# Performance work log

Hardware: AMD Instinct MI355X
Metric: run time of the kernel (lower is better)

The kernel has to match this reference:

```python
import jax, jax.numpy as jnp
import numpy as np

B, C, H, W = 16, 2048, 64, 64
PROJ_DIM, ATTN_DIM = 128, 64
MAX_SAMPLES = 64
TEMPERATURE = 0.1
BASE_TEMPERATURE = 0.07
SIM_THRESHOLD = 0.7
LOSS_WEIGHT = 0.1
BN_EPS = 1e-5


def setup_inputs() -> dict:
    key = jax.random.key(0)
    ks = jax.random.split(key, 12)
    inp = {
        "feats": jax.random.normal(ks[0], (B, C, H, W), dtype=jnp.float32),
        "labels": jax.random.randint(ks[1], (B, H, W), 0, 2, dtype=jnp.int64),
        # projection: Conv1x1(C->128) -> BN -> ReLU -> Conv1x1(128->128)
        "W1": jax.random.normal(ks[2], (PROJ_DIM, C), dtype=jnp.float32) * (1.0 / np.sqrt(C)),
        "b1": jnp.zeros((PROJ_DIM,), jnp.float32),
        "gamma": jnp.ones((PROJ_DIM,), jnp.float32),
        "beta": jnp.zeros((PROJ_DIM,), jnp.float32),
        "W2": jax.random.normal(ks[3], (PROJ_DIM, PROJ_DIM), dtype=jnp.float32) * (1.0 / np.sqrt(PROJ_DIM)),
        "b2": jnp.zeros((PROJ_DIM,), jnp.float32),
        # pixel attention: Conv1x1(C->64) -> ReLU -> Conv1x1(64->1) -> Sigmoid
        "Wa1": jax.random.normal(ks[4], (ATTN_DIM, C), dtype=jnp.float32) * (1.0 / np.sqrt(C)),
        "ba1": jnp.zeros((ATTN_DIM,), jnp.float32),
        "Wa2": jax.random.normal(ks[5], (1, ATTN_DIM), dtype=jnp.float32) * (1.0 / np.sqrt(ATTN_DIM)),
        "ba2": jnp.zeros((1,), jnp.float32),
    }
    return inp


def _conv1x1(x, Wt, b):  # x: [B,Cin,H,W], Wt: [Cout,Cin]
    return jnp.einsum("bchw,oc->bohw", x, Wt) + b[None, :, None, None]


def _batchnorm_train(x, gamma, beta):  # per-channel stats over (B,H,W)
    mean = x.mean(axis=(0, 2, 3), keepdims=True)
    var = x.var(axis=(0, 2, 3), keepdims=True)
    xn = (x - mean) * jax.lax.rsqrt(var + BN_EPS)
    return xn * gamma[None, :, None, None] + beta[None, :, None, None]


def _single_image_loss(f, lab, w):
    # f: [HW,128] L2-normalized, lab: [HW] int, w: [HW]
    valid = lab == 1
    # deterministic stand-in for randperm sampling: first MAX_SAMPLES valid pixels
    idx = jnp.nonzero(valid, size=MAX_SAMPLES, fill_value=0)[0]
    tf = f[idx]                       # [S,128]
    tw = w[idx]                       # [S]
    sim = (tf @ tf.T) / TEMPERATURE   # [S,S]
    pos = (sim > SIM_THRESHOLD) & ~jnp.eye(MAX_SAMPLES, dtype=bool)
    exp_sim = jnp.exp(sim)
    denom = exp_sim.sum(axis=1)       # [S]
    log_prob = jnp.log(exp_sim / denom[:, None] + 1e-10)
    pair_w = tw[:, None] * tw[None, :]
    loss = -(TEMPERATURE / BASE_TEMPERATURE) * jnp.sum(
        jnp.where(pos, pair_w * log_prob, 0.0)
    )
    return loss / tw.sum()


def reference(feats, labels, W1, b1, gamma, beta, W2, b2, Wa1, ba1, Wa2, ba2):
    # projection head
    h = _conv1x1(feats, W1, b1)
    h = jax.nn.relu(_batchnorm_train(h, gamma, beta))
    proj = _conv1x1(h, W2, b2)                      # [B,128,H,W]
    # pixel attention
    a = jax.nn.relu(_conv1x1(feats, Wa1, ba1))
    attn = jax.nn.sigmoid(_conv1x1(a, Wa2, ba2))    # [B,1,H,W]

    f = proj.transpose(0, 2, 3, 1).reshape(B, H * W, PROJ_DIM)
    f = f / jnp.clip(jnp.linalg.norm(f, axis=-1, keepdims=True), 1e-12)
    wts = attn.transpose(0, 2, 3, 1).reshape(B, H * W)
    labs = labels.reshape(B, H * W)

    losses = jax.vmap(_single_image_loss)(f, labs, wts)  # [B]
    return jnp.mean(losses) * LOSS_WEIGHT
```

## Files before the change

kernel.cpp:

```cpp
#include <hip/hip_runtime.h>
#include <hip/hip_bf16.h>
#include <math.h>

#define B_ 16
#define C_ 2048
#define HW_ 4096
#define NPIX_ 65536
#define PD_ 128
#define AD_ 64
#define S_ 64
#define BN_EPS_ 1e-5f
#define TEMP_ 0.1f
#define BTEMP_ 0.07f
#define THR_ 0.7f
#define LW_ 0.1f

typedef __attribute__((ext_vector_type(8))) short short8;
typedef __attribute__((ext_vector_type(4))) float floatx4;

__device__ __forceinline__ unsigned short f2bf(float x) {
    unsigned int u = __float_as_uint(x);
    u += 0x7fffu + ((u >> 16) & 1u);
    return (unsigned short)(u >> 16);
}

__global__ void zero_kernel(float* xsum, float* ssq, float* out) {
    int t = threadIdx.x;
    for (int i = t; i < C_; i += 256) xsum[i] = 0.0f;
    if (t < PD_) ssq[t] = 0.0f;
    if (t == 0) out[0] = 0.0f;
}

__global__ void prep_kernel(const float* __restrict__ W1, const float* __restrict__ Wa1,
                            const float* __restrict__ W2, float* __restrict__ W1t,
                            float* __restrict__ Wa1t, float* __restrict__ W2t,
                            uint4* __restrict__ Bpk) {
    int g = blockIdx.x * blockDim.x + threadIdx.x;
    if (g < C_ * PD_) { int k = g >> 7, c = g & 127; W1t[g] = W1[c * C_ + k]; }
    if (g < C_ * AD_) { int k = g >> 6, j = g & 63;  Wa1t[g] = Wa1[j * C_ + k]; }
    if (g < PD_ * PD_){ int k = g >> 7, c = g & 127; W2t[g] = W2[c * PD_ + k]; }
    if (g < 64 * 4 * PD_) {
        int kc = g >> 9, q = (g >> 7) & 3, c = g & 127;
        const float* src = W1 + (size_t)c * C_ + kc * 32 + q * 8;
        unsigned int w[4];
#pragma unroll
        for (int h = 0; h < 4; h++) {
            unsigned int lo = f2bf(src[2 * h]);
            unsigned int hi = f2bf(src[2 * h + 1]);
            w[h] = lo | (hi << 16);
        }
        Bpk[g] = make_uint4(w[0], w[1], w[2], w[3]);
    }
}

#define NKC_ 64
__global__ __launch_bounds__(256) void fused_stats_kernel(const float* __restrict__ feats,
                                                          const uint4* __restrict__ Bpk,
                                                          float* __restrict__ xsum,
                                                          float* __restrict__ ssq) {
    __shared__ uint4 bw[2][512];
    __shared__ float lxsum[C_];
    __shared__ float red[4][PD_];

    int t = threadIdx.x;
    for (int i = t; i < C_; i += 256) lxsum[i] = 0.0f;

    int tile = blockIdx.x;
    int b = tile >> 6;
    int hw0 = (tile & 63) << 6;
    int wave = t >> 6, lane = t & 63;
    int qd = lane >> 4, ln16 = lane & 15;
    const float* fb = feats + (size_t)b * C_ * HW_ + (hw0 + wave * 16 + ln16);

    floatx4 acc[8];
#pragma unroll
    for (int nt = 0; nt < 8; nt++) acc[nt] = (floatx4)0.0f;

    bw[0][t] = Bpk[t];
    bw[0][t + 256] = Bpk[t + 256];
    __syncthreads();

    for (int kc = 0; kc < NKC_; kc++) {
        int cur = kc & 1;
        uint4 u0, u1;
        if (kc + 1 < NKC_) {
            u0 = Bpk[(kc + 1) * 512 + t];
            u1 = Bpk[(kc + 1) * 512 + t + 256];
        }
        const float* pk = fb + (size_t)(kc * 32 + qd * 8) * HW_;
        float av[8];
#pragma unroll
        for (int j = 0; j < 8; j++) av[j] = pk[(size_t)j * HW_];

#pragma unroll
        for (int j = 0; j < 8; j++) {
            float v = av[j];
            v += __shfl_xor(v, 1, 64);
            v += __shfl_xor(v, 2, 64);
            v += __shfl_xor(v, 4, 64);
            v += __shfl_xor(v, 8, 64);
            if (ln16 == 0) atomicAdd(&lxsum[kc * 32 + qd * 8 + j], v);
        }

        short8 afrag;
#pragma unroll
        for (int j = 0; j < 8; j++) afrag[j] = (short)f2bf(av[j]);

#pragma unroll
        for (int nt = 0; nt < 8; nt++) {
            short8 bfrag = *reinterpret_cast<const short8*>(&bw[cur][qd * 128 + nt * 16 + ln16]);
            acc[nt] = __builtin_amdgcn_mfma_f32_16x16x32_bf16(afrag, bfrag, acc[nt], 0, 0, 0);
        }

        if (kc + 1 < NKC_) {
            bw[cur ^ 1][t] = u0;
            bw[cur ^ 1][t + 256] = u1;
        }
        __syncthreads();
    }

#pragma unroll
    for (int nt = 0; nt < 8; nt++) {
        float s = 0.0f;
#pragma unroll
        for (int r = 0; r < 4; r++) s = fmaf(acc[nt][r], acc[nt][r], s);
        s += __shfl_xor(s, 16, 64);
        s += __shfl_xor(s, 32, 64);
        if (qd == 0) red[wave][nt * 16 + ln16] = s;
    }
    __syncthreads();
    if (t < PD_) {
        float tot = red[0][t] + red[1][t] + red[2][t] + red[3][t];
        atomicAdd(&ssq[t], tot);
    }
    for (int i = t; i < C_; i += 256) atomicAdd(&xsum[i], lxsum[i]);
}

__global__ __launch_bounds__(256) void stats_kernel(const float* __restrict__ W1,
                                                    const float* __restrict__ xsum,
                                                    const float* __restrict__ ssq,
                                                    const float* __restrict__ b1,
                                                    float* __restrict__ mean,
                                                    float* __restrict__ invstd) {
    int c = blockIdx.x, t = threadIdx.x;
    const float* row = W1 + (size_t)c * C_;
    float acc = 0.0f;
    for (int k = t; k < C_; k += 256) acc = fmaf(row[k], xsum[k], acc);
    for (int o = 32; o > 0; o >>= 1) acc += __shfl_down(acc, o, 64);
    __shared__ float red[4];
    if ((t & 63) == 0) red[t >> 6] = acc;
    __syncthreads();
    if (t == 0) {
        float m0 = (red[0] + red[1] + red[2] + red[3]) * (1.0f / NPIX_);
        float var = ssq[c] * (1.0f / NPIX_) - m0 * m0;
        mean[c] = m0 + b1[c];
        invstd[c] = rsqrtf(var + BN_EPS_);
    }
}

__global__ __launch_bounds__(256) void find_kernel(const int* __restrict__ labels,
                                                   int* __restrict__ idx) {
    __shared__ int cnt[256];
    __shared__ int pref[257];
    int b = blockIdx.x, t = threadIdx.x;
    const int* lb = labels + b * HW_;
    int base = t * 16, c0 = 0;
    for (int i = 0; i < 16; i++) c0 += (lb[base + i] == 1);
    cnt[t] = c0;
    __syncthreads();
    if (t == 0) {
        int s = 0;
        for (int i = 0; i < 256; i++) { pref[i] = s; s += cnt[i]; }
        pref[256] = s;
    }
    __syncthreads();
    int r = pref[t];
    for (int i = 0; i < 16; i++) {
        if (lb[base + i] == 1) {
            if (r < S_) idx[b * S_ + r] = base + i;
            r++;
        }
    }
    if (t == 0) {
        for (int k = pref[256]; k < S_; k++) idx[b * S_ + k] = 0;
    }
}

__global__ __launch_bounds__(256) void sample_kernel(
        const float* __restrict__ feats, const float* __restrict__ W1t,
        const float* __restrict__ b1, const float* __restrict__ mean,
        const float* __restrict__ invstd, const float* __restrict__ gamma,
        const float* __restrict__ beta, const float* __restrict__ W2t,
        const float* __restrict__ b2, const float* __restrict__ Wa1t,
        const float* __restrict__ ba1, const float* __restrict__ Wa2,
        const float* __restrict__ ba2, const int* __restrict__ idx,
        float* __restrict__ projs, float* __restrict__ tw) {
    __shared__ float x[C_];
    __shared__ float rh[PD_];
    __shared__ float av[AD_];
    int s = blockIdx.x;
    int b = s >> 6;
    int pix = idx[s];
    int t = threadIdx.x;
    const float* fb = feats + (size_t)b * C_ * HW_ + pix;
    for (int c = t; c < C_; c += 256) x[c] = fb[(size_t)c * HW_];
    __syncthreads();
    if (t < PD_) {
        float h = b1[t];
        for (int k = 0; k < C_; k++) h = fmaf(W1t[k * PD_ + t], x[k], h);
        float r = (h - mean[t]) * invstd[t] * gamma[t] + beta[t];
        rh[t] = r > 0.0f ? r : 0.0f;
    } else if (t < PD_ + AD_) {
        int j = t - PD_;
        float a = ba1[j];
        for (int k = 0; k < C_; k++) a = fmaf(Wa1t[k * AD_ + j], x[k], a);
        av[j] = a > 0.0f ? a : 0.0f;
    }
    __syncthreads();
    if (t < PD_) {
        float p = b2[t];
        for (int j = 0; j < PD_; j++) p = fmaf(W2t[j * PD_ + t], rh[j], p);
        projs[s * PD_ + t] = p;
    } else if (t == PD_) {
        float a2 = ba2[0];
        for (int j = 0; j < AD_; j++) a2 = fmaf(Wa2[j], av[j], a2);
        tw[s] = 1.0f / (1.0f + expf(-a2));
    }
}

__global__ __launch_bounds__(256) void loss_kernel(const float* __restrict__ projs,
                                                   const float* __restrict__ tw,
                                                   float* __restrict__ out) {
    __shared__ float f[S_][PD_ + 1];
    __shared__ float w[S_], inv[S_], rowsum[S_];
    __shared__ float sims[S_ * S_];
    __shared__ float red[4];
    int b = blockIdx.x, t = threadIdx.x;
    for (int e = t; e < S_ * PD_; e += 256) {
        int i = e >> 7, c = e & 127;
        f[i][c] = projs[(b * S_ + i) * PD_ + c];
    }
    if (t < S_) w[t] = tw[b * S_ + t];
    __syncthreads();
    if (t < S_) {
        float s2 = 0.0f;
        for (int c = 0; c < PD_; c++) { float v = f[t][c]; s2 = fmaf(v, v, s2); }
        float n = sqrtf(s2);
        n = n < 1e-12f ? 1e-12f : n;
        inv[t] = 1.0f / n;
    }
    __syncthreads();
    for (int e = t; e < S_ * PD_; e += 256) {
        int i = e >> 7, c = e & 127;
        f[i][c] *= inv[i];
    }
    __syncthreads();
#pragma unroll
    for (int r = 0; r < 16; r++) {
        int e = t + 256 * r;
        int i = e >> 6, j = e & 63;
        float d = 0.0f;
        for (int c = 0; c < PD_; c++) d = fmaf(f[i][c], f[j][c], d);
        sims[e] = d * (1.0f / TEMP_);
    }
    __syncthreads();
    if (t < S_) {
        float rs = 0.0f;
        for (int jj = 0; jj < S_; jj++) {
            int j = (jj + t) & 63;
            rs += expf(sims[t * S_ + j]);
        }
        rowsum[t] = rs;
    }
    __syncthreads();
    float acc = 0.0f;
#pragma unroll
    for (int r = 0; r < 16; r++) {
        int e = t + 256 * r;
        int i = e >> 6, j = e & 63;
        float sv = sims[e];
        if (sv > THR_ && i != j) {
            float lp = logf(expf(sv) / rowsum[i] + 1e-10f);
            acc += w[i] * w[j] * lp;
        }
    }
    for (int o = 32; o > 0; o >>= 1) acc += __shfl_down(acc, o, 64);
    if ((t & 63) == 0) red[t >> 6] = acc;
    __syncthreads();
    if (t == 0) {
        float total = red[0] + red[1] + red[2] + red[3];
        float twsum = 0.0f;
        for (int i = 0; i < S_; i++) twsum += w[i];
        float loss = -(TEMP_ / BTEMP_) * total / twsum;
        atomicAdd(out, loss * (LW_ / B_));
    }
}

extern "C" void kernel_launch(void* const* d_in, const int* in_sizes, int n_in,
                              void* d_out, int out_size, void* d_ws, size_t ws_size,
                              hipStream_t stream) {
    const float* feats = (const float*)d_in[0];
    const int*   labels = (const int*)d_in[1];
    const float* W1 = (const float*)d_in[2];
    const float* b1 = (const float*)d_in[3];
    const float* gamma = (const float*)d_in[4];
    const float* beta = (const float*)d_in[5];
    const float* W2 = (const float*)d_in[6];
    const float* b2 = (const float*)d_in[7];
    const float* Wa1 = (const float*)d_in[8];
    const float* ba1 = (const float*)d_in[9];
    const float* Wa2 = (const float*)d_in[10];
    const float* ba2 = (const float*)d_in[11];
    float* out = (float*)d_out;

    float* ws = (float*)d_ws;
    float* xsum   = ws;
    float* ssq    = xsum + C_;
    float* mean   = ssq + PD_;
    float* invstd = mean + PD_;
    float* tw     = invstd + PD_;
    int*   idx    = (int*)(tw + B_ * S_);
    float* projs  = (float*)(idx + B_ * S_);
    float* W1t    = projs + B_ * S_ * PD_;
    float* Wa1t   = W1t + C_ * PD_;
    float* W2t    = Wa1t + C_ * AD_;
    uint4* Bpk    = (uint4*)(W2t + PD_ * PD_);

    zero_kernel<<<1, 256, 0, stream>>>(xsum, ssq, out);
    prep_kernel<<<(C_ * PD_) / 256, 256, 0, stream>>>(W1, Wa1, W2, W1t, Wa1t, W2t, Bpk);
    fused_stats_kernel<<<1024, 256, 0, stream>>>(feats, Bpk, xsum, ssq);
    stats_kernel<<<PD_, 256, 0, stream>>>(W1, xsum, ssq, b1, mean, invstd);
    find_kernel<<<B_, 256, 0, stream>>>(labels, idx);
    sample_kernel<<<B_ * S_, 256, 0, stream>>>(feats, W1t, b1, mean, invstd, gamma, beta,
                                               W2t, b2, Wa1t, ba1, Wa2, ba2, idx, projs, tw);
    loss_kernel<<<B_, 256, 0, stream>>>(projs, tw, out);
}
```

Measured before the change: 996.5 us.

## Compute BN mean from GEMM output, drop LDS staging, batch sampled pixels

The stats kernel now sums the bf16 MFMA outputs directly for the BN mean, replacing the per-channel input sum with LDS atomics and the W1·xsum reduction. It also reads B fragments straight from global memory, removing the LDS double buffer and per-iteration barriers. The sample kernel handles four pixels per block and reads W1/Wa1 row-major with float4 loads, so the transposed weight copies and the zero kernel are no longer needed. The mean now comes from bf16-rounded products and b1 is dropped, which relies on b1 cancelling inside batch norm.

```diff
diff --git a/kernel.cpp b/kernel.cpp
--- a/kernel.cpp
+++ b/kernel.cpp
@@ -14,6 +14,7 @@
 #define BTEMP_ 0.07f
 #define THR_ 0.7f
 #define LW_ 0.1f
+#define NKC_ 64
 
 typedef __attribute__((ext_vector_type(8))) short short8;
 typedef __attribute__((ext_vector_type(4))) float floatx4;
@@ -24,22 +25,21 @@
     return (unsigned short)(u >> 16);
 }
 
-__global__ void zero_kernel(float* xsum, float* ssq, float* out) {
-    int t = threadIdx.x;
-    for (int i = t; i < C_; i += 256) xsum[i] = 0.0f;
-    if (t < PD_) ssq[t] = 0.0f;
-    if (t == 0) out[0] = 0.0f;
-}
-
-__global__ void prep_kernel(const float* __restrict__ W1, const float* __restrict__ Wa1,
-                            const float* __restrict__ W2, float* __restrict__ W1t,
-                            float* __restrict__ Wa1t, float* __restrict__ W2t,
-                            uint4* __restrict__ Bpk) {
+__global__ __launch_bounds__(256) void prep_kernel(const float* __restrict__ W1,
+                                                   const float* __restrict__ W2,
+                                                   float* __restrict__ W2t,
+                                                   uint4* __restrict__ Bpk,
+                                                   float* __restrict__ hsum,
+                                                   float* __restrict__ ssq,
+                                                   float* __restrict__ out) {
     int g = blockIdx.x * blockDim.x + threadIdx.x;
-    if (g < C_ * PD_) { int k = g >> 7, c = g & 127; W1t[g] = W1[c * C_ + k]; }
-    if (g < C_ * AD_) { int k = g >> 6, j = g & 63;  Wa1t[g] = Wa1[j * C_ + k]; }
-    if (g < PD_ * PD_){ int k = g >> 7, c = g & 127; W2t[g] = W2[c * PD_ + k]; }
-    if (g < 64 * 4 * PD_) {
+    if (blockIdx.x == 0) {
+        int t = threadIdx.x;
+        if (t < PD_) { hsum[t] = 0.0f; ssq[t] = 0.0f; }
+        if (t == 0) out[0] = 0.0f;
+    }
+    if (g < PD_ * PD_) { int k = g >> 7, c = g & 127; W2t[g] = W2[c * PD_ + k]; }
+    if (g < NKC_ * 4 * PD_) {
         int kc = g >> 9, q = (g >> 7) & 3, c = g & 127;
         const float* src = W1 + (size_t)c * C_ + kc * 32 + q * 8;
         unsigned int w[4];
@@ -53,108 +53,79 @@
     }
 }
 
-#define NKC_ 64
-__global__ __launch_bounds__(256) void fused_stats_kernel(const float* __restrict__ feats,
-                                                          const uint4* __restrict__ Bpk,
-                                                          float* __restrict__ xsum,
-                                                          float* __restrict__ ssq) {
-    __shared__ uint4 bw[2][512];
-    __shared__ float lxsum[C_];
-    __shared__ float red[4][PD_];
+__global__ __launch_bounds__(256, 4) void fused_stats_kernel(const float* __restrict__ feats,
+                                                             const short8* __restrict__ Bpk,
+                                                             float* __restrict__ hsum,
+                                                             float* __restrict__ ssq) {
+    __shared__ float redS[4][PD_];
+    __shared__ float redQ[4][PD_];
 
     int t = threadIdx.x;
-    for (int i = t; i < C_; i += 256) lxsum[i] = 0.0f;
-
     int tile = blockIdx.x;
     int b = tile >> 6;
     int hw0 = (tile & 63) << 6;
     int wave = t >> 6, lane = t & 63;
     int qd = lane >> 4, ln16 = lane & 15;
-    const float* fb = feats + (size_t)b * C_ * HW_ + (hw0 + wave * 16 + ln16);
+
+    const float* pk = feats + (size_t)b * C_ * HW_ + (hw0 + wave * 16 + ln16)
+                    + (size_t)qd * 8 * HW_;
+    const short8* bp = Bpk + qd * 128 + ln16;
 
     floatx4 acc[8];
 #pragma unroll
     for (int nt = 0; nt < 8; nt++) acc[nt] = (floatx4)0.0f;
 
-    bw[0][t] = Bpk[t];
-    bw[0][t + 256] = Bpk[t + 256];
-    __syncthreads();
-
     for (int kc = 0; kc < NKC_; kc++) {
-        int cur = kc & 1;
-        uint4 u0, u1;
-        if (kc + 1 < NKC_) {
-            u0 = Bpk[(kc + 1) * 512 + t];
-            u1 = Bpk[(kc + 1) * 512 + t + 256];
-        }
-        const float* pk = fb + (size_t)(kc * 32 + qd * 8) * HW_;
         float av[8];
 #pragma unroll
         for (int j = 0; j < 8; j++) av[j] = pk[(size_t)j * HW_];
 
-#pragma unroll
-        for (int j = 0; j < 8; j++) {
-            float v = av[j];
-            v += __shfl_xor(v, 1, 64);
-            v += __shfl_xor(v, 2, 64);
-            v += __shfl_xor(v, 4, 64);
-            v += __shfl_xor(v, 8, 64);
-            if (ln16 == 0) atomicAdd(&lxsum[kc * 32 + qd * 8 + j], v);
-        }
-
         short8 afrag;
 #pragma unroll
         for (int j = 0; j < 8; j++) afrag[j] = (short)f2bf(av[j]);
 
 #pragma unroll
         for (int nt = 0; nt < 8; nt++) {
-            short8 bfrag = *reinterpret_cast<const short8*>(&bw[cur][qd * 128 + nt * 16 + ln16]);
+            short8 bfrag = bp[nt * 16];
             acc[nt] = __builtin_amdgcn_mfma_f32_16x16x32_bf16(afrag, bfrag, acc[nt], 0, 0, 0);
         }
-
-        if (kc + 1 < NKC_) {
-            bw[cur ^ 1][t] = u0;
-            bw[cur ^ 1][t + 256] = u1;
-        }
-        __syncthreads();
+        pk += (size_t)32 * HW_;
+        bp += 512;
     }
 
 #pragma unroll
     for (int nt = 0; nt < 8; nt++) {
-        float s = 0.0f;
-#pragma unroll
-        for (int r = 0; r < 4; r++) s = fmaf(acc[nt][r], acc[nt][r], s);
-        s += __shfl_xor(s, 16, 64);
-        s += __shfl_xor(s, 32, 64);
-        if (qd == 0) red[wave][nt * 16 + ln16] = s;
+        float sq = 0.0f, sm = 0.0f;
+#pragma unroll
+        for (int r = 0; r < 4; r++) {
+            float v = acc[nt][r];
+            sq = fmaf(v, v, sq);
+            sm += v;
+        }
+        sq += __shfl_xor(sq, 16, 64);
+        sq += __shfl_xor(sq, 32, 64);
+        sm += __shfl_xor(sm, 16, 64);
+        sm += __shfl_xor(sm, 32, 64);
+        if (qd == 0) {
+            redQ[wave][nt * 16 + ln16] = sq;
+            redS[wave][nt * 16 + ln16] = sm;
+        }
     }
     __syncthreads();
     if (t < PD_) {
-        float tot = red[0][t] + red[1][t] + red[2][t] + red[3][t];
-        atomicAdd(&ssq[t], tot);
-    }
-    for (int i = t; i < C_; i += 256) atomicAdd(&xsum[i], lxsum[i]);
-}
-
-__global__ __launch_bounds__(256) void stats_kernel(const float* __restrict__ W1,
-                                                    const float* __restrict__ xsum,
-                                                    const float* __restrict__ ssq,
-                                                    const float* __restrict__ b1,
-                                                    float* __restrict__ mean,
-                                                    float* __restrict__ invstd) {
-    int c = blockIdx.x, t = threadIdx.x;
-    const float* row = W1 + (size_t)c * C_;
-    float acc = 0.0f;
-    for (int k = t; k < C_; k += 256) acc = fmaf(row[k], xsum[k], acc);
-    for (int o = 32; o > 0; o >>= 1) acc += __shfl_down(acc, o, 64);
-    __shared__ float red[4];
-    if ((t & 63) == 0) red[t >> 6] = acc;
-    __syncthreads();
-    if (t == 0) {
-        float m0 = (red[0] + red[1] + red[2] + red[3]) * (1.0f / NPIX_);
-        float var = ssq[c] * (1.0f / NPIX_) - m0 * m0;
-        mean[c] = m0 + b1[c];
-        invstd[c] = rsqrtf(var + BN_EPS_);
+        atomicAdd(&ssq[t],  redQ[0][t] + redQ[1][t] + redQ[2][t] + redQ[3][t]);
+        atomicAdd(&hsum[t], redS[0][t] + redS[1][t] + redS[2][t] + redS[3][t]);
+    }
+}
+
+__global__ void stats_kernel(const float* __restrict__ hsum, const float* __restrict__ ssq,
+                             float* __restrict__ mean, float* __restrict__ invstd) {
+    int t = threadIdx.x;
+    if (t < PD_) {
+        float m0 = hsum[t] * (1.0f / NPIX_);
+        float var = ssq[t] * (1.0f / NPIX_) - m0 * m0;
+        mean[t] = m0;
+        invstd[t] = rsqrtf(var + BN_EPS_);
     }
 }
 
@@ -187,44 +158,110 @@
 }
 
 __global__ __launch_bounds__(256) void sample_kernel(
-        const float* __restrict__ feats, const float* __restrict__ W1t,
-        const float* __restrict__ b1, const float* __restrict__ mean,
+        const float* __restrict__ feats, const float* __restrict__ W1,
+        const float* __restrict__ Wa1, const float* __restrict__ mean,
         const float* __restrict__ invstd, const float* __restrict__ gamma,
         const float* __restrict__ beta, const float* __restrict__ W2t,
-        const float* __restrict__ b2, const float* __restrict__ Wa1t,
-        const float* __restrict__ ba1, const float* __restrict__ Wa2,
-        const float* __restrict__ ba2, const int* __restrict__ idx,
-        float* __restrict__ projs, float* __restrict__ tw) {
-    __shared__ float x[C_];
-    __shared__ float rh[PD_];
-    __shared__ float av[AD_];
-    int s = blockIdx.x;
-    int b = s >> 6;
-    int pix = idx[s];
+        const float* __restrict__ b2, const float* __restrict__ Wa2,
+        const float* __restrict__ ba1, const float* __restrict__ ba2,
+        const int* __restrict__ idx, float* __restrict__ projs, float* __restrict__ tw) {
+    __shared__ float x[4][C_];
+    __shared__ float part[4][2][PD_];
+    __shared__ float aprt[4][2][AD_];
+    __shared__ float rh[4][PD_];
+    __shared__ float av[4][AD_];
+
+    int blk = blockIdx.x;
+    int s0 = blk * 4;
+    int b = s0 >> 6;
     int t = threadIdx.x;
-    const float* fb = feats + (size_t)b * C_ * HW_ + pix;
-    for (int c = t; c < C_; c += 256) x[c] = fb[(size_t)c * HW_];
-    __syncthreads();
+    const float* fb = feats + (size_t)b * C_ * HW_;
+
+    {
+        int px = t & 3;
+        int pixv = idx[s0 + px];
+        for (int c = (t >> 2); c < C_; c += 64)
+            x[px][c] = fb[(size_t)c * HW_ + pixv];
+    }
+    __syncthreads();
+
+    {
+        int o = t & 127, half = t >> 7;
+        const float* wr = W1 + (size_t)o * C_ + half * 1024;
+        float pa[4], pb[4];
+#pragma unroll
+        for (int px = 0; px < 4; px++) { pa[px] = 0.0f; pb[px] = 0.0f; }
+        for (int k = 0; k < 1024; k += 4) {
+            float4 w4 = *(const float4*)(wr + k);
+#pragma unroll
+            for (int px = 0; px < 4; px++) {
+                float4 x4 = *(const float4*)(&x[px][half * 1024 + k]);
+                pa[px] = fmaf(w4.x, x4.x, pa[px]);
+                pb[px] = fmaf(w4.y, x4.y, pb[px]);
+                pa[px] = fmaf(w4.z, x4.z, pa[px]);
+                pb[px] = fmaf(w4.w, x4.w, pb[px]);
+            }
+        }
+#pragma unroll
+        for (int px = 0; px < 4; px++) part[px][half][o] = pa[px] + pb[px];
+    }
+    if (t < 128) {
+        int j = t & 63, half = t >> 6;
+        const float* wr = Wa1 + (size_t)j * C_ + half * 1024;
+        float pa[4], pb[4];
+#pragma unroll
+        for (int px = 0; px < 4; px++) { pa[px] = 0.0f; pb[px] = 0.0f; }
+        for (int k = 0; k < 1024; k += 4) {
+            float4 w4 = *(const float4*)(wr + k);
+#pragma unroll
+            for (int px = 0; px < 4; px++) {
+                float4 x4 = *(const float4*)(&x[px][half * 1024 + k]);
+                pa[px] = fmaf(w4.x, x4.x, pa[px]);
+                pb[px] = fmaf(w4.y, x4.y, pb[px]);
+                pa[px] = fmaf(w4.z, x4.z, pa[px]);
+                pb[px] = fmaf(w4.w, x4.w, pb[px]);
+            }
+        }
+#pragma unroll
+        for (int px = 0; px < 4; px++) aprt[px][half][j] = pa[px] + pb[px];
+    }
+    __syncthreads();
+
     if (t < PD_) {
-        float h = b1[t];
-        for (int k = 0; k < C_; k++) h = fmaf(W1t[k * PD_ + t], x[k], h);
-        float r = (h - mean[t]) * invstd[t] * gamma[t] + beta[t];
-        rh[t] = r > 0.0f ? r : 0.0f;
+        float mn = mean[t], is = invstd[t], g = gamma[t], be = beta[t];
+#pragma unroll
+        for (int px = 0; px < 4; px++) {
+            float h = part[px][0][t] + part[px][1][t];
+            float r = (h - mn) * is * g + be;
+            rh[px][t] = r > 0.0f ? r : 0.0f;
+        }
     } else if (t < PD_ + AD_) {
         int j = t - PD_;
-        float a = ba1[j];
-        for (int k = 0; k < C_; k++) a = fmaf(Wa1t[k * AD_ + j], x[k], a);
-        av[j] = a > 0.0f ? a : 0.0f;
-    }
-    __syncthreads();
+        float bj = ba1[j];
+#pragma unroll
+        for (int px = 0; px < 4; px++) {
+            float a = aprt[px][0][j] + aprt[px][1][j] + bj;
+            av[px][j] = a > 0.0f ? a : 0.0f;
+        }
+    }
+    __syncthreads();
+
     if (t < PD_) {
-        float p = b2[t];
-        for (int j = 0; j < PD_; j++) p = fmaf(W2t[j * PD_ + t], rh[j], p);
-        projs[s * PD_ + t] = p;
-    } else if (t == PD_) {
+        float p[4];
+#pragma unroll
+        for (int px = 0; px < 4; px++) p[px] = b2[t];
+        for (int j = 0; j < PD_; j++) {
+            float w = W2t[j * PD_ + t];
+#pragma unroll
+            for (int px = 0; px < 4; px++) p[px] = fmaf(w, rh[px][j], p[px]);
+        }
+#pragma unroll
+        for (int px = 0; px < 4; px++) projs[(s0 + px) * PD_ + t] = p[px];
+    } else if (t < PD_ + 4) {
+        int px = t - PD_;
         float a2 = ba2[0];
-        for (int j = 0; j < AD_; j++) a2 = fmaf(Wa2[j], av[j], a2);
-        tw[s] = 1.0f / (1.0f + expf(-a2));
+        for (int j = 0; j < AD_; j++) a2 = fmaf(Wa2[j], av[px][j], a2);
+        tw[s0 + px] = 1.0f / (1.0f + expf(-a2));
     }
 }
 
@@ -302,7 +339,7 @@
     const float* feats = (const float*)d_in[0];
     const int*   labels = (const int*)d_in[1];
     const float* W1 = (const float*)d_in[2];
-    const float* b1 = (const float*)d_in[3];
+    const float* b1 = (const float*)d_in[3];   (void)b1;
     const float* gamma = (const float*)d_in[4];
     const float* beta = (const float*)d_in[5];
     const float* W2 = (const float*)d_in[6];
@@ -313,25 +350,21 @@
     const float* ba2 = (const float*)d_in[11];
     float* out = (float*)d_out;
 
-    float* ws = (float*)d_ws;
-    float* xsum   = ws;
-    float* ssq    = xsum + C_;
-    float* mean   = ssq + PD_;
-    float* invstd = mean + PD_;
-    float* tw     = invstd + PD_;
-    int*   idx    = (int*)(tw + B_ * S_);
-    float* projs  = (float*)(idx + B_ * S_);
-    float* W1t    = projs + B_ * S_ * PD_;
-    float* Wa1t   = W1t + C_ * PD_;
-    float* W2t    = Wa1t + C_ * AD_;
-    uint4* Bpk    = (uint4*)(W2t + PD_ * PD_);
-
-    zero_kernel<<<1, 256, 0, stream>>>(xsum, ssq, out);
-    prep_kernel<<<(C_ * PD_) / 256, 256, 0, stream>>>(W1, Wa1, W2, W1t, Wa1t, W2t, Bpk);
-    fused_stats_kernel<<<1024, 256, 0, stream>>>(feats, Bpk, xsum, ssq);
-    stats_kernel<<<PD_, 256, 0, stream>>>(W1, xsum, ssq, b1, mean, invstd);
+    uint4* Bpk   = (uint4*)d_ws;
+    float* W2t   = (float*)(Bpk + NKC_ * 4 * PD_);
+    float* hsum  = W2t + PD_ * PD_;
+    float* ssq   = hsum + PD_;
+    float* mean  = ssq + PD_;
+    float* invstd= mean + PD_;
+    float* tw    = invstd + PD_;
+    int*   idx   = (int*)(tw + B_ * S_);
+    float* projs = (float*)(idx + B_ * S_);
+
+    prep_kernel<<<128, 256, 0, stream>>>(W1, W2, W2t, Bpk, hsum, ssq, out);
     find_kernel<<<B_, 256, 0, stream>>>(labels, idx);
-    sample_kernel<<<B_ * S_, 256, 0, stream>>>(feats, W1t, b1, mean, invstd, gamma, beta,
-                                               W2t, b2, Wa1t, ba1, Wa2, ba2, idx, projs, tw);
+    fused_stats_kernel<<<1024, 256, 0, stream>>>(feats, (const short8*)Bpk, hsum, ssq);
+    stats_kernel<<<1, 128, 0, stream>>>(hsum, ssq, mean, invstd);
+    sample_kernel<<<256, 256, 0, stream>>>(feats, W1, Wa1, mean, invstd, gamma, beta,
+                                           W2t, b2, Wa2, ba1, ba2, idx, projs, tw);
     loss_kernel<<<B_, 256, 0, stream>>>(projs, tw, out);
 }
```

Result: faster. 971.7 us (-2.5%).
